# Performance work log

Measured on AMD Instinct MI355X. Metric: run time of the kernel, lower is better.

Reference implementation:

```python
import jax, jax.numpy as jnp
import numpy as np

N = 4096
D = 512   # d_model == dff (required by the original code path)
H = 4
NEG = -1e10
ALPHA = 0.3  # keras LeakyReLU default alpha


def setup_inputs() -> dict:
    key = jax.random.key(0)
    ks = jax.random.split(key, 8)
    nodes = jax.random.normal(ks[0], (N, D), dtype=jnp.float32)
    # sparse-ish 0/1 dense adjacency with self loops
    adj = (jax.random.uniform(ks[1], (N, N)) < 0.01).astype(jnp.float32)
    adj = jnp.maximum(adj, jnp.eye(N, dtype=jnp.float32))
    s = 0.05
    W_node = jax.random.normal(ks[2], (D, D), dtype=jnp.float32) * s
    b_node = jnp.zeros((D,), dtype=jnp.float32)
    K = jax.random.normal(ks[3], (H, D, D), dtype=jnp.float32) * s
    A_self = jax.random.normal(ks[4], (H, D), dtype=jnp.float32) * s
    A_neigh = jax.random.normal(ks[5], (H, D), dtype=jnp.float32) * s
    return {"nodes": nodes, "adj": adj, "W_node": W_node, "b_node": b_node,
            "K": K, "A_self": A_self, "A_neigh": A_neigh, "num_heads": H}


def reference(nodes, adj, W_node, b_node, K, A_self, A_neigh, num_heads):
    # node_layer: Dense(dff)
    x = nodes @ W_node + b_node                       # [N, D]
    # per-head projection, vectorized over heads
    feats = jnp.einsum('nd,hdf->hnf', x, K)           # [H, N, D]
    # additive attention scores; both terms are per-row scalars -> [H, N]
    s = jnp.einsum('hnf,hf->hn', feats, A_self) + jnp.einsum('hnf,hf->hn', feats, A_neigh)
    s = jnp.where(s > 0, s, ALPHA * s)                # LeakyReLU(alpha=0.3)
    # broadcast row score over columns + adjacency mask, softmax over neighbors
    logits = s[:, :, None] + NEG * (1.0 - adj)[None]  # [H, N, N]
    attn = jax.nn.softmax(logits, axis=-1)
    # dropout is identity at inference (training=False)
    out = jnp.einsum('hij,hjf->hif', attn, feats)     # [H, N, D]
    out = jnp.mean(out, axis=0)                       # mean over heads
    return jax.nn.relu(out)
```

## Files before the change

kernel.cpp:

```cpp
#include <hip/hip_runtime.h>


typedef short  short8 __attribute__((ext_vector_type(8)));
typedef float  f32x4  __attribute__((ext_vector_type(4)));

__device__ inline unsigned short f2bf(float f) {
    union { float f; unsigned int u; } v; v.f = f;
    unsigned int u = v.u;
    u += 0x7fffu + ((u >> 16) & 1u);
    return (unsigned short)(u >> 16);
}

__device__ inline void gl_lds16(const void* gp, void* lp) {
    __builtin_amdgcn_global_load_lds(
        (const __attribute__((address_space(1))) void*)gp,
        (__attribute__((address_space(3))) void*)lp, 16, 0, 0);
}

__global__ __launch_bounds__(512, 4) void prep_kernel(
        const float* __restrict__ nodes, const float* __restrict__ adj,
        const float* __restrict__ W, const float* __restrict__ b,
        const float* __restrict__ K,
        unsigned short* __restrict__ MmatT, float* __restrict__ bias2,
        unsigned short* __restrict__ nodesBf,
        int* __restrict__ degArr, int* __restrict__ nbrArr,
        int N, int D, int H, int numCast) {
    __shared__ union {
        struct {
            unsigned short As[2][64][40];
            unsigned short Bs[2][64][40];
        } g;
        float red64[64][64];
        int   lst[1024];
    } sm;
    __shared__ float red2[8][64];
    __shared__ int cnt;

    const int bid = blockIdx.x;
    const int tid = threadIdx.x;
    const int DD  = D * D;
    const int lane = tid & 63, wave = tid >> 6;
    const int l15 = lane & 15, quad = lane >> 4;

    if (bid < 64) {
        const int by = bid >> 3, bx = bid & 7;
        const int f0 = by * 64, d0 = bx * 64;
        const float invH = 1.0f / (float)H;
        const int h  = tid >> 8;
        const int th = tid & 255;
        const int wy = (wave >> 1) & 1, wx = wave & 1;
        const int kk = th >> 3;
        const int ff = (th & 7) * 8;
        const int dr = th >> 2;
        const int dk = (th & 3) * 8;
        const int kh = h * 256;

        f32x4 acc[2][2] = {};
        for (int k0 = 0; k0 < 256; k0 += 32) {
            f32x4 kv[4][2];
#pragma unroll
            for (int hh = 0; hh < 4; ++hh) {
                const float* kp = K + ((size_t)hh * D + (kh + k0 + kk)) * D + f0 + ff;
                kv[hh][0] = *reinterpret_cast<const f32x4*>(kp);
                kv[hh][1] = *reinterpret_cast<const f32x4*>(kp + 4);
            }
            const float* wp = W + (size_t)(d0 + dr) * D + kh + k0 + dk;
            f32x4 wu = *reinterpret_cast<const f32x4*>(wp);
            f32x4 wv = *reinterpret_cast<const f32x4*>(wp + 4);

            float s[8];
#pragma unroll
            for (int j = 0; j < 4; ++j) {
                s[j]     = kv[0][0][j] + kv[1][0][j] + kv[2][0][j] + kv[3][0][j];
                s[j + 4] = kv[0][1][j] + kv[1][1][j] + kv[2][1][j] + kv[3][1][j];
            }
            short8 bv;
#pragma unroll
            for (int j = 0; j < 4; ++j) {
                bv[j]     = (short)f2bf(wu[j]);
                bv[j + 4] = (short)f2bf(wv[j]);
            }
            __syncthreads();
#pragma unroll
            for (int j = 0; j < 8; ++j)
                sm.g.As[h][ff + j][kk] = f2bf(s[j] * invH);
            *reinterpret_cast<short8*>(&sm.g.Bs[h][dr][dk]) = bv;
            __syncthreads();
            short8 a0 = *reinterpret_cast<const short8*>(&sm.g.As[h][wy * 32 +      l15][quad * 8]);
            short8 a1 = *reinterpret_cast<const short8*>(&sm.g.As[h][wy * 32 + 16 + l15][quad * 8]);
            short8 b0 = *reinterpret_cast<const short8*>(&sm.g.Bs[h][wx * 32 +      l15][quad * 8]);
            short8 b1 = *reinterpret_cast<const short8*>(&sm.g.Bs[h][wx * 32 + 16 + l15][quad * 8]);
            acc[0][0] = __builtin_amdgcn_mfma_f32_16x16x32_bf16(a0, b0, acc[0][0], 0, 0, 0);
            acc[0][1] = __builtin_amdgcn_mfma_f32_16x16x32_bf16(a0, b1, acc[0][1], 0, 0, 0);
            acc[1][0] = __builtin_amdgcn_mfma_f32_16x16x32_bf16(a1, b0, acc[1][0], 0, 0, 0);
            acc[1][1] = __builtin_amdgcn_mfma_f32_16x16x32_bf16(a1, b1, acc[1][1], 0, 0, 0);
        }
        __syncthreads();
        if (h == 1) {
#pragma unroll
            for (int mi = 0; mi < 2; ++mi)
#pragma unroll
                for (int ni = 0; ni < 2; ++ni)
#pragma unroll
                    for (int r = 0; r < 4; ++r)
                        sm.red64[wy * 32 + mi * 16 + quad * 4 + r]
                                [wx * 32 + ni * 16 + l15] = acc[mi][ni][r];
        }
        __syncthreads();
        if (h == 0) {
#pragma unroll
            for (int mi = 0; mi < 2; ++mi)
#pragma unroll
                for (int ni = 0; ni < 2; ++ni) {
                    int col = d0 + wx * 32 + ni * 16 + l15;
#pragma unroll
                    for (int r = 0; r < 4; ++r) {
                        int row = f0 + wy * 32 + mi * 16 + quad * 4 + r;
                        float v = acc[mi][ni][r] +
                            sm.red64[wy * 32 + mi * 16 + quad * 4 + r]
                                    [wx * 32 + ni * 16 + l15];
                        MmatT[(size_t)row * D + col] = f2bf(v);
                    }
                }
        }
    } else if (bid < 72) {
        const int f0 = (bid - 64) * 64;
        const int fl = tid & 63, grp = tid >> 6;
        const float invH = 1.0f / (float)H;
        float a = 0.f;
        for (int d0i = grp * 64; d0i < grp * 64 + 64; d0i += 4) {
            float v[4] = {0.f, 0.f, 0.f, 0.f};
#pragma unroll
            for (int dd = 0; dd < 4; ++dd)
#pragma unroll
                for (int hh = 0; hh < 4; ++hh)
                    v[dd] += K[((size_t)hh * D + d0i + dd) * D + f0 + fl];
#pragma unroll
            for (int dd = 0; dd < 4; ++dd) a += b[d0i + dd] * v[dd];
        }
        red2[grp][fl] = a;
        __syncthreads();
        if (tid < 64) {
            float s = 0.f;
#pragma unroll
            for (int gg = 0; gg < 8; ++gg) s += red2[gg][tid];
            bias2[f0 + tid] = s * invH;
        }
    } else if (bid < 72 + N) {
        const int row = bid - 72;
        if (tid == 0) cnt = 0;
        __syncthreads();
        const f32x4* ap = reinterpret_cast<const f32x4*>(adj + (size_t)row * N + tid * 8);
        f32x4 av[2];
        av[0] = ap[0];
        av[1] = ap[1];
#pragma unroll
        for (int c = 0; c < 2; ++c) {
            int b4 = tid * 8 + c * 4;
#pragma unroll
            for (int j = 0; j < 4; ++j)
                if (av[c][j] > 0.5f) {
                    int p = atomicAdd(&cnt, 1);
                    if (p < 1024) sm.lst[p] = b4 + j;
                }
        }
        __syncthreads();
        int deg = cnt; if (deg > 1024) deg = 1024;
        if (tid == 0) degArr[row] = deg;
        for (int i = tid; i < deg; i += 512)
            nbrArr[(size_t)row * 1024 + i] = sm.lst[i];
    } else {
        const int total  = (N * D) >> 3;
        const int stride = numCast << 9;
        for (int i = (bid - 72 - N) * 512 + tid; i < total; i += stride) {
            const float* p = nodes + (size_t)i * 8;
            f32x4 x = *reinterpret_cast<const f32x4*>(p);
            f32x4 y = *reinterpret_cast<const f32x4*>(p + 4);
            short8 o;
#pragma unroll
            for (int j = 0; j < 4; ++j) {
                o[j]     = (short)f2bf(x[j]);
                o[j + 4] = (short)f2bf(y[j]);
            }
            *reinterpret_cast<short8*>(nodesBf + (size_t)i * 8) = o;
        }
    }
}

__global__ __launch_bounds__(256) void gemm2_kernel(
        const unsigned short* __restrict__ nodesBf,
        const unsigned short* __restrict__ MmatT,
        const float* __restrict__ bias2, unsigned short* __restrict__ g, int D) {
    __shared__ unsigned short As[2][64][32];
    __shared__ unsigned short Bs[2][64][32];
    const int bid = blockIdx.x;
    const int lb = (bid & 7) * 64 + (bid >> 3);
    const int by = lb >> 3, bx = lb & 7;
    const int tid = threadIdx.x;
    const int lane = tid & 63, wave = tid >> 6;
    const int wy = wave >> 1, wx = wave & 1;
    const int l15 = lane & 15, quad = lane >> 4;

    const int cgl = ((tid & 3) ^ ((tid >> 3) & 3)) * 8;
    const unsigned short* Ag = nodesBf + (size_t)(by * 64 + (tid >> 2)) * D + cgl;
    const unsigned short* Bg = MmatT   + (size_t)(bx * 64 + (tid >> 2)) * D + cgl;
    unsigned short* AsW0 = &As[0][0][0] + wave * 512;
    unsigned short* AsW1 = &As[1][0][0] + wave * 512;
    unsigned short* BsW0 = &Bs[0][0][0] + wave * 512;
    unsigned short* BsW1 = &Bs[1][0][0] + wave * 512;

    f32x4 acc[2][2] = {};
    gl_lds16(Ag, AsW0);
    gl_lds16(Bg, BsW0);

    const int ra = wy * 32 + l15, rb = wx * 32 + l15;
    const int qa = (quad ^ ((ra >> 1) & 3)) * 8;
    const int qb = (quad ^ ((rb >> 1) & 3)) * 8;

    int cur = 0;
#pragma unroll
    for (int k0 = 0; k0 < 512; k0 += 32) {
        if (k0 + 32 < 512) {
            gl_lds16(Ag + k0 + 32, cur ? AsW0 : AsW1);
            gl_lds16(Bg + k0 + 32, cur ? BsW0 : BsW1);
            asm volatile("s_waitcnt vmcnt(2)" ::: "memory");
        } else {
            asm volatile("s_waitcnt vmcnt(0)" ::: "memory");
        }
        __builtin_amdgcn_s_barrier();
        __builtin_amdgcn_sched_barrier(0);
        const unsigned short* Af = cur ? &As[1][0][0] : &As[0][0][0];
        const unsigned short* Bf = cur ? &Bs[1][0][0] : &Bs[0][0][0];
        short8 a0 = *reinterpret_cast<const short8*>(Af + (ra     ) * 32 + qa);
        short8 a1 = *reinterpret_cast<const short8*>(Af + (ra + 16) * 32 + qa);
        short8 b0 = *reinterpret_cast<const short8*>(Bf + (rb     ) * 32 + qb);
        short8 b1 = *reinterpret_cast<const short8*>(Bf + (rb + 16) * 32 + qb);
        acc[0][0] = __builtin_amdgcn_mfma_f32_16x16x32_bf16(a0, b0, acc[0][0], 0, 0, 0);
        acc[0][1] = __builtin_amdgcn_mfma_f32_16x16x32_bf16(a0, b1, acc[0][1], 0, 0, 0);
        acc[1][0] = __builtin_amdgcn_mfma_f32_16x16x32_bf16(a1, b0, acc[1][0], 0, 0, 0);
        acc[1][1] = __builtin_amdgcn_mfma_f32_16x16x32_bf16(a1, b1, acc[1][1], 0, 0, 0);
        __builtin_amdgcn_sched_barrier(0);
        asm volatile("s_waitcnt lgkmcnt(0)" ::: "memory");
        __builtin_amdgcn_s_barrier();
        cur ^= 1;
    }

#pragma unroll
    for (int mi = 0; mi < 2; ++mi)
#pragma unroll
        for (int ni = 0; ni < 2; ++ni) {
            int col = bx * 64 + wx * 32 + ni * 16 + l15;
            float bvl = bias2[col];
#pragma unroll
            for (int r = 0; r < 4; ++r) {
                int row = by * 64 + wy * 32 + mi * 16 + quad * 4 + r;
                g[(size_t)row * D + col] = f2bf(acc[mi][ni][r] + bvl);
            }
        }
}

__global__ __launch_bounds__(256) void aggregate_kernel(
        const int* __restrict__ degArr, const int* __restrict__ nbrArr,
        const unsigned short* __restrict__ g, float* __restrict__ out,
        int N, int D) {
    const int row = blockIdx.x;
    const int tid = threadIdx.x;
    __shared__ int lst[1024];
    const int deg = degArr[row];
    for (int i = tid; i < deg; i += 256) lst[i] = nbrArr[(size_t)row * 1024 + i];
    __syncthreads();

    const int col = tid * 2;
    float acc0 = 0.f, acc1 = 0.f;
    int k = 0;
    for (; k + 8 <= deg; k += 8) {
        unsigned int u[8];
#pragma unroll
        for (int j = 0; j < 8; ++j)
            u[j] = *reinterpret_cast<const unsigned int*>(&g[(size_t)lst[k + j] * D + col]);
#pragma unroll
        for (int j = 0; j < 8; ++j) {
            union { unsigned int i; float f; } lo, hi;
            lo.i = u[j] << 16; hi.i = u[j] & 0xffff0000u;
            acc0 += lo.f; acc1 += hi.f;
        }
    }
    for (; k < deg; ++k) {
        unsigned int u = *reinterpret_cast<const unsigned int*>(&g[(size_t)lst[k] * D + col]);
        union { unsigned int i; float f; } lo, hi;
        lo.i = u << 16; hi.i = u & 0xffff0000u;
        acc0 += lo.f; acc1 += hi.f;
    }

    float inv = deg > 0 ? 1.f / (float)deg : 0.f;
    acc0 *= inv; acc1 *= inv;
    float2 o;
    o.x = acc0 > 0.f ? acc0 : 0.f;
    o.y = acc1 > 0.f ? acc1 : 0.f;
    *reinterpret_cast<float2*>(&out[(size_t)row * D + col]) = o;
}

extern "C" void kernel_launch(void* const* d_in, const int* in_sizes, int n_in,
                              void* d_out, int out_size, void* d_ws, size_t ws_size,
                              hipStream_t stream) {
    const float* nodes  = (const float*)d_in[0];
    const float* adj    = (const float*)d_in[1];
    const float* W_node = (const float*)d_in[2];
    const float* b_node = (const float*)d_in[3];
    const float* K      = (const float*)d_in[4];

    const int D  = in_sizes[3];
    const int N  = in_sizes[0] / D;
    const int H  = in_sizes[4] / (D * D);
    const int DD = D * D;

    float* out = (float*)d_out;

    char* ws = (char*)d_ws;
    unsigned short* MmatT   = (unsigned short*)(ws);
    size_t off = (size_t)DD * 2;
    float*          bias2   = (float*)(ws + off);          off += (size_t)D * 4;
    unsigned short* nodesBf = (unsigned short*)(ws + off); off += (size_t)N * D * 2;
    unsigned short* g_bf16  = (unsigned short*)(ws + off); off += (size_t)N * D * 2;
    int*            degArr  = (int*)(ws + off);            off += (size_t)N * 4;
    int*            nbrArr  = (int*)(ws + off);

    const int numCast = 512;
    prep_kernel<<<dim3(64 + 8 + N + numCast), 512, 0, stream>>>(
        nodes, adj, W_node, b_node, K, MmatT, bias2, nodesBf, degArr, nbrArr,
        N, D, H, numCast);

    gemm2_kernel<<<dim3((N / 64) * (D / 64)), 256, 0, stream>>>(
        nodesBf, MmatT, bias2, g_bf16, D);

    aggregate_kernel<<<dim3(N), 256, 0, stream>>>(degArr, nbrArr, g_bf16, out, N, D);
}
```

Before: 148.7 us.

## Move adjacency scan from prep kernel into GEMM launch to overlap

The adjacency-row scan that builds neighbor lists moves out of the prep kernel and into the second launch, running alongside the GEMM blocks. The prep kernel now only builds the fused weight matrix, the bias and the bf16 cast of nodes, so the GEMM's dependencies finish sooner. The scan then overlaps with the GEMM in one launch, using 256 threads per row with 16 elements each. The shared memory is a union of the GEMM tiles and the neighbor list. The GEMM blocks now share the GPU with 4096 memory-bound scan blocks, which could slow the GEMM.

Measured after the change: 152.6 us. 2.7% more time.

```diff
diff --git a/kernel.cpp b/kernel.cpp
--- a/kernel.cpp
+++ b/kernel.cpp
@@ -17,13 +17,12 @@
         (__attribute__((address_space(3))) void*)lp, 16, 0, 0);
 }
 
-__global__ __launch_bounds__(512, 4) void prep_kernel(
-        const float* __restrict__ nodes, const float* __restrict__ adj,
+__global__ __launch_bounds__(512, 4) void prep0_kernel(
+        const float* __restrict__ nodes,
         const float* __restrict__ W, const float* __restrict__ b,
         const float* __restrict__ K,
         unsigned short* __restrict__ MmatT, float* __restrict__ bias2,
         unsigned short* __restrict__ nodesBf,
-        int* __restrict__ degArr, int* __restrict__ nbrArr,
         int N, int D, int H, int numCast) {
     __shared__ union {
         struct {
@@ -31,10 +30,8 @@
             unsigned short Bs[2][64][40];
         } g;
         float red64[64][64];
-        int   lst[1024];
     } sm;
     __shared__ float red2[8][64];
-    __shared__ int cnt;
 
     const int bid = blockIdx.x;
     const int tid = threadIdx.x;
@@ -146,17 +143,116 @@
             for (int gg = 0; gg < 8; ++gg) s += red2[gg][tid];
             bias2[f0 + tid] = s * invH;
         }
-    } else if (bid < 72 + N) {
-        const int row = bid - 72;
+    } else {
+        const int total  = (N * D) >> 3;
+        const int stride = numCast << 9;
+        for (int i = (bid - 72) * 512 + tid; i < total; i += stride) {
+            const float* p = nodes + (size_t)i * 8;
+            f32x4 x = *reinterpret_cast<const f32x4*>(p);
+            f32x4 y = *reinterpret_cast<const f32x4*>(p + 4);
+            short8 o;
+#pragma unroll
+            for (int j = 0; j < 4; ++j) {
+                o[j]     = (short)f2bf(x[j]);
+                o[j + 4] = (short)f2bf(y[j]);
+            }
+            *reinterpret_cast<short8*>(nodesBf + (size_t)i * 8) = o;
+        }
+    }
+}
+
+__global__ __launch_bounds__(256) void scan_gemm_kernel(
+        const unsigned short* __restrict__ nodesBf,
+        const unsigned short* __restrict__ MmatT,
+        const float* __restrict__ bias2, unsigned short* __restrict__ g,
+        const float* __restrict__ adj,
+        int* __restrict__ degArr, int* __restrict__ nbrArr, int N, int D) {
+    __shared__ union {
+        struct {
+            unsigned short As[2][64][32];
+            unsigned short Bs[2][64][32];
+        } t;
+        int lst[1024];
+    } sm;
+    __shared__ int cnt;
+
+    const int bid = blockIdx.x;
+    const int tid = threadIdx.x;
+
+    if (bid < 512) {
+        const int lb = (bid & 7) * 64 + (bid >> 3);
+        const int by = lb >> 3, bx = lb & 7;
+        const int lane = tid & 63, wave = tid >> 6;
+        const int wy = wave >> 1, wx = wave & 1;
+        const int l15 = lane & 15, quad = lane >> 4;
+
+        const int cgl = ((tid & 3) ^ ((tid >> 3) & 3)) * 8;
+        const unsigned short* Ag = nodesBf + (size_t)(by * 64 + (tid >> 2)) * D + cgl;
+        const unsigned short* Bg = MmatT   + (size_t)(bx * 64 + (tid >> 2)) * D + cgl;
+        unsigned short* AsW0 = &sm.t.As[0][0][0] + wave * 512;
+        unsigned short* AsW1 = &sm.t.As[1][0][0] + wave * 512;
+        unsigned short* BsW0 = &sm.t.Bs[0][0][0] + wave * 512;
+        unsigned short* BsW1 = &sm.t.Bs[1][0][0] + wave * 512;
+
+        f32x4 acc[2][2] = {};
+        gl_lds16(Ag, AsW0);
+        gl_lds16(Bg, BsW0);
+
+        const int ra = wy * 32 + l15, rb = wx * 32 + l15;
+        const int qa = (quad ^ ((ra >> 1) & 3)) * 8;
+        const int qb = (quad ^ ((rb >> 1) & 3)) * 8;
+
+        int cur = 0;
+#pragma unroll
+        for (int k0 = 0; k0 < 512; k0 += 32) {
+            if (k0 + 32 < 512) {
+                gl_lds16(Ag + k0 + 32, cur ? AsW0 : AsW1);
+                gl_lds16(Bg + k0 + 32, cur ? BsW0 : BsW1);
+                asm volatile("s_waitcnt vmcnt(2)" ::: "memory");
+            } else {
+                asm volatile("s_waitcnt vmcnt(0)" ::: "memory");
+            }
+            __builtin_amdgcn_s_barrier();
+            __builtin_amdgcn_sched_barrier(0);
+            const unsigned short* Af = cur ? &sm.t.As[1][0][0] : &sm.t.As[0][0][0];
+            const unsigned short* Bf = cur ? &sm.t.Bs[1][0][0] : &sm.t.Bs[0][0][0];
+            short8 a0 = *reinterpret_cast<const short8*>(Af + (ra     ) * 32 + qa);
+            short8 a1 = *reinterpret_cast<const short8*>(Af + (ra + 16) * 32 + qa);
+            short8 b0 = *reinterpret_cast<const short8*>(Bf + (rb     ) * 32 + qb);
+            short8 b1 = *reinterpret_cast<const short8*>(Bf + (rb + 16) * 32 + qb);
+            acc[0][0] = __builtin_amdgcn_mfma_f32_16x16x32_bf16(a0, b0, acc[0][0], 0, 0, 0);
+            acc[0][1] = __builtin_amdgcn_mfma_f32_16x16x32_bf16(a0, b1, acc[0][1], 0, 0, 0);
+            acc[1][0] = __builtin_amdgcn_mfma_f32_16x16x32_bf16(a1, b0, acc[1][0], 0, 0, 0);
+            acc[1][1] = __builtin_amdgcn_mfma_f32_16x16x32_bf16(a1, b1, acc[1][1], 0, 0, 0);
+            __builtin_amdgcn_sched_barrier(0);
+            asm volatile("s_waitcnt lgkmcnt(0)" ::: "memory");
+            __builtin_amdgcn_s_barrier();
+            cur ^= 1;
+        }
+
+#pragma unroll
+        for (int mi = 0; mi < 2; ++mi)
+#pragma unroll
+            for (int ni = 0; ni < 2; ++ni) {
+                int col = bx * 64 + wx * 32 + ni * 16 + l15;
+                float bvl = bias2[col];
+#pragma unroll
+                for (int r = 0; r < 4; ++r) {
+                    int row = by * 64 + wy * 32 + mi * 16 + quad * 4 + r;
+                    g[(size_t)row * D + col] = f2bf(acc[mi][ni][r] + bvl);
+                }
+            }
+    } else {
+        const int row = bid - 512;
         if (tid == 0) cnt = 0;
         __syncthreads();
-        const f32x4* ap = reinterpret_cast<const f32x4*>(adj + (size_t)row * N + tid * 8);
-        f32x4 av[2];
-        av[0] = ap[0];
-        av[1] = ap[1];
-#pragma unroll
-        for (int c = 0; c < 2; ++c) {
-            int b4 = tid * 8 + c * 4;
+        const f32x4* ap = reinterpret_cast<const f32x4*>(adj + (size_t)row * N + tid * 16);
+        f32x4 av[4];
+#pragma unroll
+        for (int c = 0; c < 4; ++c) av[c] = ap[c];
+#pragma unroll
+        for (int c = 0; c < 4; ++c) {
+            int b4 = tid * 16 + c * 4;
 #pragma unroll
             for (int j = 0; j < 4; ++j)
                 if (av[c][j] > 0.5f) {
@@ -167,96 +263,9 @@
         __syncthreads();
         int deg = cnt; if (deg > 1024) deg = 1024;
         if (tid == 0) degArr[row] = deg;
-        for (int i = tid; i < deg; i += 512)
+        for (int i = tid; i < deg; i += 256)
             nbrArr[(size_t)row * 1024 + i] = sm.lst[i];
-    } else {
-        const int total  = (N * D) >> 3;
-        const int stride = numCast << 9;
-        for (int i = (bid - 72 - N) * 512 + tid; i < total; i += stride) {
-            const float* p = nodes + (size_t)i * 8;
-            f32x4 x = *reinterpret_cast<const f32x4*>(p);
-            f32x4 y = *reinterpret_cast<const f32x4*>(p + 4);
-            short8 o;
-#pragma unroll
-            for (int j = 0; j < 4; ++j) {
-                o[j]     = (short)f2bf(x[j]);
-                o[j + 4] = (short)f2bf(y[j]);
-            }
-            *reinterpret_cast<short8*>(nodesBf + (size_t)i * 8) = o;
-        }
     }
-}
-
-__global__ __launch_bounds__(256) void gemm2_kernel(
-        const unsigned short* __restrict__ nodesBf,
-        const unsigned short* __restrict__ MmatT,
-        const float* __restrict__ bias2, unsigned short* __restrict__ g, int D) {
-    __shared__ unsigned short As[2][64][32];
-    __shared__ unsigned short Bs[2][64][32];
-    const int bid = blockIdx.x;
-    const int lb = (bid & 7) * 64 + (bid >> 3);
-    const int by = lb >> 3, bx = lb & 7;
-    const int tid = threadIdx.x;
-    const int lane = tid & 63, wave = tid >> 6;
-    const int wy = wave >> 1, wx = wave & 1;
-    const int l15 = lane & 15, quad = lane >> 4;
-
-    const int cgl = ((tid & 3) ^ ((tid >> 3) & 3)) * 8;
-    const unsigned short* Ag = nodesBf + (size_t)(by * 64 + (tid >> 2)) * D + cgl;
-    const unsigned short* Bg = MmatT   + (size_t)(bx * 64 + (tid >> 2)) * D + cgl;
-    unsigned short* AsW0 = &As[0][0][0] + wave * 512;
-    unsigned short* AsW1 = &As[1][0][0] + wave * 512;
-    unsigned short* BsW0 = &Bs[0][0][0] + wave * 512;
-    unsigned short* BsW1 = &Bs[1][0][0] + wave * 512;
-
-    f32x4 acc[2][2] = {};
-    gl_lds16(Ag, AsW0);
-    gl_lds16(Bg, BsW0);
-
-    const int ra = wy * 32 + l15, rb = wx * 32 + l15;
-    const int qa = (quad ^ ((ra >> 1) & 3)) * 8;
-    const int qb = (quad ^ ((rb >> 1) & 3)) * 8;
-
-    int cur = 0;
-#pragma unroll
-    for (int k0 = 0; k0 < 512; k0 += 32) {
-        if (k0 + 32 < 512) {
-            gl_lds16(Ag + k0 + 32, cur ? AsW0 : AsW1);
-            gl_lds16(Bg + k0 + 32, cur ? BsW0 : BsW1);
-            asm volatile("s_waitcnt vmcnt(2)" ::: "memory");
-        } else {
-            asm volatile("s_waitcnt vmcnt(0)" ::: "memory");
-        }
-        __builtin_amdgcn_s_barrier();
-        __builtin_amdgcn_sched_barrier(0);
-        const unsigned short* Af = cur ? &As[1][0][0] : &As[0][0][0];
-        const unsigned short* Bf = cur ? &Bs[1][0][0] : &Bs[0][0][0];
-        short8 a0 = *reinterpret_cast<const short8*>(Af + (ra     ) * 32 + qa);
-        short8 a1 = *reinterpret_cast<const short8*>(Af + (ra + 16) * 32 + qa);
-        short8 b0 = *reinterpret_cast<const short8*>(Bf + (rb     ) * 32 + qb);
-        short8 b1 = *reinterpret_cast<const short8*>(Bf + (rb + 16) * 32 + qb);
-        acc[0][0] = __builtin_amdgcn_mfma_f32_16x16x32_bf16(a0, b0, acc[0][0], 0, 0, 0);
-        acc[0][1] = __builtin_amdgcn_mfma_f32_16x16x32_bf16(a0, b1, acc[0][1], 0, 0, 0);
-        acc[1][0] = __builtin_amdgcn_mfma_f32_16x16x32_bf16(a1, b0, acc[1][0], 0, 0, 0);
-        acc[1][1] = __builtin_amdgcn_mfma_f32_16x16x32_bf16(a1, b1, acc[1][1], 0, 0, 0);
-        __builtin_amdgcn_sched_barrier(0);
-        asm volatile("s_waitcnt lgkmcnt(0)" ::: "memory");
-        __builtin_amdgcn_s_barrier();
-        cur ^= 1;
-    }
-
-#pragma unroll
-    for (int mi = 0; mi < 2; ++mi)
-#pragma unroll
-        for (int ni = 0; ni < 2; ++ni) {
-            int col = bx * 64 + wx * 32 + ni * 16 + l15;
-            float bvl = bias2[col];
-#pragma unroll
-            for (int r = 0; r < 4; ++r) {
-                int row = by * 64 + wy * 32 + mi * 16 + quad * 4 + r;
-                g[(size_t)row * D + col] = f2bf(acc[mi][ni][r] + bvl);
-            }
-        }
 }
 
 __global__ __launch_bounds__(256) void aggregate_kernel(
@@ -326,12 +335,11 @@
     int*            nbrArr  = (int*)(ws + off);
 
     const int numCast = 512;
-    prep_kernel<<<dim3(64 + 8 + N + numCast), 512, 0, stream>>>(
-        nodes, adj, W_node, b_node, K, MmatT, bias2, nodesBf, degArr, nbrArr,
-        N, D, H, numCast);
-
-    gemm2_kernel<<<dim3((N / 64) * (D / 64)), 256, 0, stream>>>(
-        nodesBf, MmatT, bias2, g_bf16, D);
+    prep0_kernel<<<dim3(64 + 8 + numCast), 512, 0, stream>>>(
+        nodes, W_node, b_node, K, MmatT, bias2, nodesBf, N, D, H, numCast);
+
+    scan_gemm_kernel<<<dim3(512 + N), 256, 0, stream>>>(
+        nodesBf, MmatT, bias2, g_bf16, adj, degArr, nbrArr, N, D);
 
     aggregate_kernel<<<dim3(N), 256, 0, stream>>>(degArr, nbrArr, g_bf16, out, N, D);
 }
```
